# Kernel tuning notes

Hardware: AMD Instinct MI355X
Metric: run time of the kernel (lower is better)

## Reference

```python
import jax, jax.numpy as jnp
import numpy as np

SL, BS, HS, FFN = 2048, 1, 512, 2048
E, TOP_K = 8, 2


def setup_inputs() -> dict:
    key = jax.random.key(0)
    k_x, k_w, k_i, k_w1, k_w2 = jax.random.split(key, 5)
    x = jax.random.normal(k_x, (SL, BS, HS), dtype=jnp.float32)
    expert_weights = jax.random.uniform(k_w, (SL * BS, TOP_K), dtype=jnp.float32)
    expert_indices = jax.random.randint(k_i, (SL * BS, TOP_K), 0, E, dtype=jnp.int32)
    # grouped expert MLP params (megablocks GroupedMLP, regular type, no bias)
    w1 = jax.random.normal(k_w1, (E, HS, FFN), dtype=jnp.float32) * (HS ** -0.5)
    w2 = jax.random.normal(k_w2, (E, FFN, HS), dtype=jnp.float32) * (FFN ** -0.5)
    return {"x": x, "expert_weights": expert_weights, "expert_indices": expert_indices,
            "w1": w1, "w2": w2}


def reference(x, expert_weights, expert_indices, w1, w2):
    sl, bs, hs = x.shape
    n_tok = sl * bs
    xf = x.reshape(n_tok, hs)                      # [N, hs]
    ew = expert_weights.reshape(-1)                # [N*top_k]
    ei = expert_indices.reshape(-1)                # [N*top_k]

    # indices_and_bins: stable radix sort of assignments by expert id
    indices = jnp.argsort(ei)                      # stable in jax -> sorted assignment ids
    bin_ids = ei[indices]                          # sorted expert id per assignment

    # megablocks gather: row for assignment i is indices[i] // top_k
    rows = indices // TOP_K                        # [T]
    xg = xf[rows]                                  # [T, hs] expert-contiguous tokens

    # grouped GEMM expert MLP (dense masked loop over fixed expert count)
    outg = jnp.zeros_like(xg)
    for e in range(E):
        m = (bin_ids == e).astype(x.dtype)[:, None]
        h = jax.nn.gelu(xg @ w1[e], approximate=False)   # [T, ffn]
        outg = outg + m * (h @ w2[e])                    # [T, hs]

    # buffer.index_add_(0, E*input_indices + bin_ids, output.detach())
    buf_idx = E * rows + bin_ids
    buffer = jnp.zeros((n_tok * E, hs), x.dtype).at[buf_idx].add(
        jax.lax.stop_gradient(outg))

    # megablocks scatter: weighted combine back to token order
    y = jnp.zeros((n_tok, hs), x.dtype).at[rows].add(outg * ew[indices][:, None])
    return y.reshape(sl, bs, hs), buffer.reshape(n_tok, E, hs)
```

## Files before the change

kernel.cpp:

```cpp
#include <hip/hip_runtime.h>
#include <hip/hip_bf16.h>

#define NTOK 2048
#define TOPK 2
#define HS   512
#define FFN  2048
#define NE   8
#define TASSIGN (NTOK*TOPK)
#define BM 64
#define PADMAX 4608
#define MAXTILES 72

typedef __attribute__((ext_vector_type(8))) short bf16x8;
typedef __attribute__((ext_vector_type(4))) float f32x4;

static const size_t OFF_XBF  = 0;
static const size_t OFF_WT   = 2097152;
static const size_t OFF_H    = 18874368;
static const size_t OFF_OUTV = 37748736;
static const size_t OFF_RT   = 47185920;
static const size_t OFF_HROF = 47204352;
static const size_t OFF_TE   = 47220736;
static const size_t OFF_TR0  = 47221056;

__device__ __forceinline__ unsigned short f2bf(float f) {
    union { __hip_bfloat16 h; unsigned short u; } v;
    v.h = __float2bfloat16(f);
    return v.u;
}

__device__ __forceinline__ int swz(int r, int byte_off) {
    return byte_off ^ ((r & 7) << 4);
}

__global__ void k_xcvt(const float* __restrict__ x, unsigned short* __restrict__ xbf) {
    int i = (blockIdx.x * 256 + threadIdx.x) * 4;
    float4 v = *(const float4*)(x + i);
    ushort4 o;
    o.x = f2bf(v.x); o.y = f2bf(v.y); o.z = f2bf(v.z); o.w = f2bf(v.w);
    *(ushort4*)(xbf + i) = o;
}

__global__ void k_transpose(const float* __restrict__ in, unsigned short* __restrict__ out,
                            int R, int C) {
    __shared__ unsigned short t[32][33];
    int e = blockIdx.z;
    int rb = blockIdx.y * 32, cb = blockIdx.x * 32;
    int tx = threadIdx.x, ty = threadIdx.y;
    const float* ip = in + (size_t)e * R * C;
    unsigned short* op = out + (size_t)e * C * R;
#pragma unroll
    for (int i = 0; i < 4; i++) {
        int r = ty + i * 8;
        t[r][tx] = f2bf(ip[(size_t)(rb + r) * C + cb + tx]);
    }
    __syncthreads();
#pragma unroll
    for (int i = 0; i < 4; i++) {
        int c = ty + i * 8;
        op[(size_t)(cb + c) * R + rb + tx] = t[tx][c];
    }
}

__global__ void k_setup(const int* __restrict__ ei, const float* __restrict__ ew,
                        int* __restrict__ rowtok, int* __restrict__ hrof,
                        int* __restrict__ tile_e, int* __restrict__ tile_r0) {
    __shared__ int cnt[NE], offpad[NE], cur[NE];
    int tid = threadIdx.x;
    for (int i = tid; i < PADMAX; i += 256) rowtok[i] = -1;
    if (tid < NE) cnt[tid] = 0;
    __syncthreads();
    for (int a = tid; a < TASSIGN; a += 256) atomicAdd(&cnt[ei[a]], 1);
    __syncthreads();
    if (tid == 0) {
        int o = 0, t = 0;
        for (int e = 0; e < NE; e++) {
            offpad[e] = o;
            cur[e] = 0;
            for (int r = 0; r < cnt[e]; r += BM) { tile_e[t] = e; tile_r0[t] = o + r; t++; }
            o += (cnt[e] + BM - 1) / BM * BM;
        }
        for (; t < MAXTILES; t++) { tile_e[t] = -1; tile_r0[t] = 0; }
    }
    __syncthreads();
    for (int a = tid; a < TASSIGN; a += 256) {
        int e = ei[a];
        int r = atomicAdd(&cur[e], 1);
        int hr = offpad[e] + r;
        rowtok[hr] = a >> 1;
        hrof[a] = hr;
    }
}

__global__ __launch_bounds__(256) void k_gemm1(
        const unsigned short* __restrict__ xbf, const unsigned short* __restrict__ w1T,
        unsigned short* __restrict__ H, const int* __restrict__ rowtok,
        const int* __restrict__ tile_e, const int* __restrict__ tile_r0) {
    int mt = blockIdx.y;
    int e = tile_e[mt];
    if (e < 0) return;
    int hr0 = tile_r0[mt];
    int ct = blockIdx.x;

    __shared__ int4 Asv[512];
    __shared__ int4 Bsv[512];
    char* As = (char*)Asv;
    char* Bs = (char*)Bsv;

    int tid = threadIdx.x;
    int lane = tid & 63, wave = tid >> 6;
    int wm = wave >> 1, wn = wave & 1;

    const char* asrc[2]; const char* bsrc[2];
    char* adst[2]; char* bdst[2];
    int atok[2];
#pragma unroll
    for (int p = 0; p < 2; p++) {
        int idx = p * 256 + tid;
        int r = idx >> 3, c8 = idx & 7;
        int token = rowtok[hr0 + r];
        atok[p] = token;
        asrc[p] = (const char*)(xbf + (size_t)(token < 0 ? 0 : token) * HS + c8 * 8);
        bsrc[p] = (const char*)(w1T + ((size_t)e * FFN + ct * 64 + r) * HS + c8 * 8);
        adst[p] = As + swz(r, r * 128 + c8 * 16);
        bdst[p] = Bs + swz(r, r * 128 + c8 * 16);
    }

    f32x4 acc[2][2] = {};
#pragma unroll 1
    for (int kt = 0; kt < HS; kt += 64) {
#pragma unroll
        for (int p = 0; p < 2; p++) {
            int4 va = make_int4(0, 0, 0, 0);
            if (atok[p] >= 0) va = *(const int4*)(asrc[p] + kt * 2);
            *(int4*)adst[p] = va;
            *(int4*)bdst[p] = *(const int4*)(bsrc[p] + kt * 2);
        }
        __syncthreads();
#pragma unroll
        for (int kk = 0; kk < 64; kk += 32) {
            bf16x8 af[2], bfr[2];
#pragma unroll
            for (int f = 0; f < 2; f++) {
                int ar = wm * 32 + f * 16 + (lane & 15);
                af[f] = *(const bf16x8*)(As + swz(ar, ar * 128 + kk * 2 + (lane >> 4) * 16));
                int bc = wn * 32 + f * 16 + (lane & 15);
                bfr[f] = *(const bf16x8*)(Bs + swz(bc, bc * 128 + kk * 2 + (lane >> 4) * 16));
            }
#pragma unroll
            for (int i = 0; i < 2; i++)
#pragma unroll
                for (int j = 0; j < 2; j++)
                    acc[i][j] = __builtin_amdgcn_mfma_f32_16x16x32_bf16(af[i], bfr[j], acc[i][j], 0, 0, 0);
        }
        __syncthreads();
    }
#pragma unroll
    for (int i = 0; i < 2; i++)
#pragma unroll
        for (int j = 0; j < 2; j++)
#pragma unroll
            for (int q = 0; q < 4; q++) {
                int row = wm * 32 + i * 16 + (lane >> 4) * 4 + q;
                int col = ct * 64 + wn * 32 + j * 16 + (lane & 15);
                float v = acc[i][j][q];
                float g = 0.5f * v * (1.0f + erff(v * 0.70710678118f));
                H[(size_t)(hr0 + row) * FFN + col] = f2bf(g);
            }
}

__global__ __launch_bounds__(256) void k_gemm2(
        const unsigned short* __restrict__ H, const unsigned short* __restrict__ w2T,
        float* __restrict__ outv,
        const int* __restrict__ tile_e, const int* __restrict__ tile_r0) {
    int mt = blockIdx.y;
    int e = tile_e[mt];
    if (e < 0) return;
    int hr0 = tile_r0[mt];
    int ct = blockIdx.x;

    __shared__ int4 Asv[512];
    __shared__ int4 Bsv[512];
    char* As = (char*)Asv;
    char* Bs = (char*)Bsv;

    int tid = threadIdx.x;
    int lane = tid & 63, wave = tid >> 6;
    int wm = wave >> 1, wn = wave & 1;

    const char* asrc[2]; const char* bsrc[2];
    char* adst[2]; char* bdst[2];
#pragma unroll
    for (int p = 0; p < 2; p++) {
        int idx = p * 256 + tid;
        int r = idx >> 3, c8 = idx & 7;
        asrc[p] = (const char*)(H + (size_t)(hr0 + r) * FFN + c8 * 8);
        bsrc[p] = (const char*)(w2T + ((size_t)e * HS + ct * 64 + r) * FFN + c8 * 8);
        adst[p] = As + swz(r, r * 128 + c8 * 16);
        bdst[p] = Bs + swz(r, r * 128 + c8 * 16);
    }

    f32x4 acc[2][2] = {};
#pragma unroll 1
    for (int kt = 0; kt < FFN; kt += 64) {
#pragma unroll
        for (int p = 0; p < 2; p++) {
            *(int4*)adst[p] = *(const int4*)(asrc[p] + kt * 2);
            *(int4*)bdst[p] = *(const int4*)(bsrc[p] + kt * 2);
        }
        __syncthreads();
#pragma unroll
        for (int kk = 0; kk < 64; kk += 32) {
            bf16x8 af[2], bfr[2];
#pragma unroll
            for (int f = 0; f < 2; f++) {
                int ar = wm * 32 + f * 16 + (lane & 15);
                af[f] = *(const bf16x8*)(As + swz(ar, ar * 128 + kk * 2 + (lane >> 4) * 16));
                int bc = wn * 32 + f * 16 + (lane & 15);
                bfr[f] = *(const bf16x8*)(Bs + swz(bc, bc * 128 + kk * 2 + (lane >> 4) * 16));
            }
#pragma unroll
            for (int i = 0; i < 2; i++)
#pragma unroll
                for (int j = 0; j < 2; j++)
                    acc[i][j] = __builtin_amdgcn_mfma_f32_16x16x32_bf16(af[i], bfr[j], acc[i][j], 0, 0, 0);
        }
        __syncthreads();
    }
#pragma unroll
    for (int i = 0; i < 2; i++)
#pragma unroll
        for (int j = 0; j < 2; j++)
#pragma unroll
            for (int q = 0; q < 4; q++) {
                int row = wm * 32 + i * 16 + (lane >> 4) * 4 + q;
                int col = ct * 64 + wn * 32 + j * 16 + (lane & 15);
                outv[(size_t)(hr0 + row) * HS + col] = acc[i][j][q];
            }
}

__global__ void k_combine(const float* __restrict__ outv, const int* __restrict__ ei,
                          const float* __restrict__ ew, const int* __restrict__ hrof,
                          float* __restrict__ y, float* __restrict__ buf) {
    int g = blockIdx.x * 256 + threadIdx.x;
    int t = g >> 9, col = g & (HS - 1);
    int a0 = 2 * t, a1 = 2 * t + 1;
    int h0 = hrof[a0], h1 = hrof[a1];
    float o0 = outv[(size_t)h0 * HS + col];
    float o1 = outv[(size_t)h1 * HS + col];
    float w0 = ew[a0], w1 = ew[a1];
    y[g] = w0 * o0 + w1 * o1;
    int e0 = ei[a0], e1 = ei[a1];
    float* bt = buf + (size_t)t * NE * HS + col;
    if (e0 == e1) {
        bt[(size_t)e0 * HS] = o0 + o1;
    } else {
        bt[(size_t)e0 * HS] = o0;
        bt[(size_t)e1 * HS] = o1;
    }
}

extern "C" void kernel_launch(void* const* d_in, const int* in_sizes, int n_in,
                              void* d_out, int out_size, void* d_ws, size_t ws_size,
                              hipStream_t stream) {
    const float* x  = (const float*)d_in[0];
    const float* ew = (const float*)d_in[1];
    const int*   ei = (const int*)d_in[2];
    const float* w1 = (const float*)d_in[3];
    const float* w2 = (const float*)d_in[4];

    char* ws = (char*)d_ws;
    unsigned short* xbf  = (unsigned short*)(ws + OFF_XBF);
    unsigned short* wT   = (unsigned short*)(ws + OFF_WT);
    unsigned short* Hb   = (unsigned short*)(ws + OFF_H);
    float*          outv = (float*)(ws + OFF_OUTV);
    int*            rowtok = (int*)(ws + OFF_RT);
    int*            hrof   = (int*)(ws + OFF_HROF);
    int*            tile_e = (int*)(ws + OFF_TE);
    int*            tile_r0= (int*)(ws + OFF_TR0);

    float* y   = (float*)d_out;
    float* buf = (float*)d_out + (size_t)NTOK * HS;

    hipMemsetAsync(d_out, 0, (size_t)out_size * sizeof(float), stream);

    k_xcvt<<<(NTOK * HS / 4 + 255) / 256, 256, 0, stream>>>(x, xbf);
    k_transpose<<<dim3(FFN / 32, HS / 32, NE), dim3(32, 8), 0, stream>>>(w1, wT, HS, FFN);
    k_setup<<<1, 256, 0, stream>>>(ei, ew, rowtok, hrof, tile_e, tile_r0);
    k_gemm1<<<dim3(FFN / 64, MAXTILES), 256, 0, stream>>>(xbf, wT, Hb, rowtok, tile_e, tile_r0);
    k_transpose<<<dim3(HS / 32, FFN / 32, NE), dim3(32, 8), 0, stream>>>(w2, wT, FFN, HS);
    k_gemm2<<<dim3(HS / 64, MAXTILES), 256, 0, stream>>>(Hb, wT, outv, tile_e, tile_r0);
    k_combine<<<NTOK * HS / 256, 256, 0, stream>>>(outv, ei, ew, hrof, y, buf);
}
```

Baseline: 104.8 us.

## Use direct global-to-LDS loads, larger GEMM tiles, and drop output memset

Merges the two grouped GEMMs into one template that loads A and B tiles straight into LDS via global_load_lds with the XOR swizzle applied on the source side. Tiles grow to 128x128 for the first GEMM and 64x128 for the second, with padding to 128 rows and separate tile lists. The output memset is removed: the combine kernel now writes all eight expert slots per token, and padded rows gather token 0 instead of zero. The two weight transposes go to separate buffers, and the workspace grows.

```diff
diff --git a/kernel.cpp b/kernel.cpp
--- a/kernel.cpp
+++ b/kernel.cpp
@@ -7,21 +7,24 @@
 #define FFN  2048
 #define NE   8
 #define TASSIGN (NTOK*TOPK)
-#define BM 64
-#define PADMAX 4608
-#define MAXTILES 72
+#define PAD  5120
+#define MAXT128 40
+#define MAXT64  72
 
 typedef __attribute__((ext_vector_type(8))) short bf16x8;
 typedef __attribute__((ext_vector_type(4))) float f32x4;
 
 static const size_t OFF_XBF  = 0;
-static const size_t OFF_WT   = 2097152;
-static const size_t OFF_H    = 18874368;
-static const size_t OFF_OUTV = 37748736;
-static const size_t OFF_RT   = 47185920;
-static const size_t OFF_HROF = 47204352;
-static const size_t OFF_TE   = 47220736;
-static const size_t OFF_TR0  = 47221056;
+static const size_t OFF_W1T  = 2097152;
+static const size_t OFF_W2T  = 18874368;
+static const size_t OFF_H    = 35651584;
+static const size_t OFF_OUTV = 56623104;
+static const size_t OFF_RT   = 67108864;
+static const size_t OFF_HROF = 67129344;
+static const size_t OFF_TE128= 67145728;
+static const size_t OFF_TR128= 67145888;
+static const size_t OFF_TE64 = 67146048;
+static const size_t OFF_TR64 = 67146336;
 
 __device__ __forceinline__ unsigned short f2bf(float f) {
     union { __hip_bfloat16 h; unsigned short u; } v;
@@ -32,6 +35,10 @@
 __device__ __forceinline__ int swz(int r, int byte_off) {
     return byte_off ^ ((r & 7) << 4);
 }
+
+#define GLOAD16(gsrc, ldst) \
+    __builtin_amdgcn_global_load_lds((const __attribute__((address_space(1))) void*)(gsrc), \
+                                     (__attribute__((address_space(3))) void*)(ldst), 16, 0, 0)
 
 __global__ void k_xcvt(const float* __restrict__ x, unsigned short* __restrict__ xbf) {
     int i = (blockIdx.x * 256 + threadIdx.x) * 4;
@@ -62,25 +69,27 @@
     }
 }
 
-__global__ void k_setup(const int* __restrict__ ei, const float* __restrict__ ew,
+__global__ void k_setup(const int* __restrict__ ei,
                         int* __restrict__ rowtok, int* __restrict__ hrof,
-                        int* __restrict__ tile_e, int* __restrict__ tile_r0) {
+                        int* __restrict__ te128, int* __restrict__ tr128,
+                        int* __restrict__ te64, int* __restrict__ tr64) {
     __shared__ int cnt[NE], offpad[NE], cur[NE];
     int tid = threadIdx.x;
-    for (int i = tid; i < PADMAX; i += 256) rowtok[i] = -1;
+    for (int i = tid; i < PAD; i += 256) rowtok[i] = 0;
     if (tid < NE) cnt[tid] = 0;
     __syncthreads();
     for (int a = tid; a < TASSIGN; a += 256) atomicAdd(&cnt[ei[a]], 1);
     __syncthreads();
     if (tid == 0) {
-        int o = 0, t = 0;
+        int o = 0, t1 = 0, t2 = 0;
         for (int e = 0; e < NE; e++) {
-            offpad[e] = o;
-            cur[e] = 0;
-            for (int r = 0; r < cnt[e]; r += BM) { tile_e[t] = e; tile_r0[t] = o + r; t++; }
-            o += (cnt[e] + BM - 1) / BM * BM;
+            offpad[e] = o; cur[e] = 0;
+            for (int r = 0; r < cnt[e]; r += 128) { te128[t1] = e; tr128[t1] = o + r; t1++; }
+            for (int r = 0; r < cnt[e]; r += 64)  { te64[t2]  = e; tr64[t2]  = o + r; t2++; }
+            o += (cnt[e] + 127) / 128 * 128;
         }
-        for (; t < MAXTILES; t++) { tile_e[t] = -1; tile_r0[t] = 0; }
+        for (; t1 < MAXT128; t1++) te128[t1] = -1;
+        for (; t2 < MAXT64;  t2++) te64[t2]  = -1;
     }
     __syncthreads();
     for (int a = tid; a < TASSIGN; a += 256) {
@@ -92,151 +101,112 @@
     }
 }
 
-__global__ __launch_bounds__(256) void k_gemm1(
-        const unsigned short* __restrict__ xbf, const unsigned short* __restrict__ w1T,
-        unsigned short* __restrict__ H, const int* __restrict__ rowtok,
-        const int* __restrict__ tile_e, const int* __restrict__ tile_r0) {
+template<int BM, int BN, int K, bool G1>
+__global__ __launch_bounds__(256) void k_gemm(
+        const unsigned short* __restrict__ A,
+        const unsigned short* __restrict__ B,
+        void* __restrict__ outp,
+        const int* __restrict__ rowtok,
+        const int* __restrict__ te, const int* __restrict__ tr) {
+    constexpr int MI = BM / 32;
+    constexpr int NJ = BN / 32;
+    constexpr int PA = BM / 32;
+    constexpr int PB = BN / 32;
     int mt = blockIdx.y;
-    int e = tile_e[mt];
+    int e = te[mt];
     if (e < 0) return;
-    int hr0 = tile_r0[mt];
+    int hr0 = tr[mt];
     int ct = blockIdx.x;
-
-    __shared__ int4 Asv[512];
-    __shared__ int4 Bsv[512];
-    char* As = (char*)Asv;
-    char* Bs = (char*)Bsv;
+    int N = gridDim.x * BN;
+
+    __shared__ unsigned short As[BM * 64];
+    __shared__ unsigned short Bs[BN * 64];
 
     int tid = threadIdx.x;
     int lane = tid & 63, wave = tid >> 6;
     int wm = wave >> 1, wn = wave & 1;
 
-    const char* asrc[2]; const char* bsrc[2];
-    char* adst[2]; char* bdst[2];
-    int atok[2];
-#pragma unroll
-    for (int p = 0; p < 2; p++) {
+    const char* asrc[PA];
+    const char* bsrc[PB];
+#pragma unroll
+    for (int p = 0; p < PA; p++) {
         int idx = p * 256 + tid;
         int r = idx >> 3, c8 = idx & 7;
-        int token = rowtok[hr0 + r];
-        atok[p] = token;
-        asrc[p] = (const char*)(xbf + (size_t)(token < 0 ? 0 : token) * HS + c8 * 8);
-        bsrc[p] = (const char*)(w1T + ((size_t)e * FFN + ct * 64 + r) * HS + c8 * 8);
-        adst[p] = As + swz(r, r * 128 + c8 * 16);
-        bdst[p] = Bs + swz(r, r * 128 + c8 * 16);
-    }
-
-    f32x4 acc[2][2] = {};
+        int c8s = c8 ^ (r & 7);
+        size_t row = G1 ? (size_t)rowtok[hr0 + r] : (size_t)(hr0 + r);
+        asrc[p] = (const char*)(A + row * K) + c8s * 16;
+    }
+#pragma unroll
+    for (int p = 0; p < PB; p++) {
+        int idx = p * 256 + tid;
+        int r = idx >> 3, c8 = idx & 7;
+        int c8s = c8 ^ (r & 7);
+        bsrc[p] = (const char*)(B + ((size_t)e * N + (size_t)ct * BN + r) * K) + c8s * 16;
+    }
+    char* aldst[PA]; char* bldst[PB];
+#pragma unroll
+    for (int p = 0; p < PA; p++) aldst[p] = (char*)As + (p * 256 + wave * 64) * 16;
+#pragma unroll
+    for (int p = 0; p < PB; p++) bldst[p] = (char*)Bs + (p * 256 + wave * 64) * 16;
+
+    f32x4 acc[MI][NJ] = {};
+
 #pragma unroll 1
-    for (int kt = 0; kt < HS; kt += 64) {
-#pragma unroll
-        for (int p = 0; p < 2; p++) {
-            int4 va = make_int4(0, 0, 0, 0);
-            if (atok[p] >= 0) va = *(const int4*)(asrc[p] + kt * 2);
-            *(int4*)adst[p] = va;
-            *(int4*)bdst[p] = *(const int4*)(bsrc[p] + kt * 2);
-        }
+    for (int kt = 0; kt < K; kt += 64) {
+#pragma unroll
+        for (int p = 0; p < PA; p++) GLOAD16(asrc[p] + kt * 2, aldst[p]);
+#pragma unroll
+        for (int p = 0; p < PB; p++) GLOAD16(bsrc[p] + kt * 2, bldst[p]);
         __syncthreads();
 #pragma unroll
         for (int kk = 0; kk < 64; kk += 32) {
-            bf16x8 af[2], bfr[2];
-#pragma unroll
-            for (int f = 0; f < 2; f++) {
-                int ar = wm * 32 + f * 16 + (lane & 15);
-                af[f] = *(const bf16x8*)(As + swz(ar, ar * 128 + kk * 2 + (lane >> 4) * 16));
-                int bc = wn * 32 + f * 16 + (lane & 15);
-                bfr[f] = *(const bf16x8*)(Bs + swz(bc, bc * 128 + kk * 2 + (lane >> 4) * 16));
+            bf16x8 af[MI], bfr[NJ];
+#pragma unroll
+            for (int i = 0; i < MI; i++) {
+                int ar = wm * (BM / 2) + i * 16 + (lane & 15);
+                af[i] = *(const bf16x8*)((const char*)As + swz(ar, ar * 128 + kk * 2 + (lane >> 4) * 16));
             }
 #pragma unroll
-            for (int i = 0; i < 2; i++)
-#pragma unroll
-                for (int j = 0; j < 2; j++)
+            for (int j = 0; j < NJ; j++) {
+                int bc = wn * (BN / 2) + j * 16 + (lane & 15);
+                bfr[j] = *(const bf16x8*)((const char*)Bs + swz(bc, bc * 128 + kk * 2 + (lane >> 4) * 16));
+            }
+#pragma unroll
+            for (int i = 0; i < MI; i++)
+#pragma unroll
+                for (int j = 0; j < NJ; j++)
                     acc[i][j] = __builtin_amdgcn_mfma_f32_16x16x32_bf16(af[i], bfr[j], acc[i][j], 0, 0, 0);
         }
         __syncthreads();
     }
-#pragma unroll
-    for (int i = 0; i < 2; i++)
-#pragma unroll
-        for (int j = 0; j < 2; j++)
-#pragma unroll
-            for (int q = 0; q < 4; q++) {
-                int row = wm * 32 + i * 16 + (lane >> 4) * 4 + q;
-                int col = ct * 64 + wn * 32 + j * 16 + (lane & 15);
-                float v = acc[i][j][q];
-                float g = 0.5f * v * (1.0f + erff(v * 0.70710678118f));
-                H[(size_t)(hr0 + row) * FFN + col] = f2bf(g);
-            }
-}
-
-__global__ __launch_bounds__(256) void k_gemm2(
-        const unsigned short* __restrict__ H, const unsigned short* __restrict__ w2T,
-        float* __restrict__ outv,
-        const int* __restrict__ tile_e, const int* __restrict__ tile_r0) {
-    int mt = blockIdx.y;
-    int e = tile_e[mt];
-    if (e < 0) return;
-    int hr0 = tile_r0[mt];
-    int ct = blockIdx.x;
-
-    __shared__ int4 Asv[512];
-    __shared__ int4 Bsv[512];
-    char* As = (char*)Asv;
-    char* Bs = (char*)Bsv;
-
-    int tid = threadIdx.x;
-    int lane = tid & 63, wave = tid >> 6;
-    int wm = wave >> 1, wn = wave & 1;
-
-    const char* asrc[2]; const char* bsrc[2];
-    char* adst[2]; char* bdst[2];
-#pragma unroll
-    for (int p = 0; p < 2; p++) {
-        int idx = p * 256 + tid;
-        int r = idx >> 3, c8 = idx & 7;
-        asrc[p] = (const char*)(H + (size_t)(hr0 + r) * FFN + c8 * 8);
-        bsrc[p] = (const char*)(w2T + ((size_t)e * HS + ct * 64 + r) * FFN + c8 * 8);
-        adst[p] = As + swz(r, r * 128 + c8 * 16);
-        bdst[p] = Bs + swz(r, r * 128 + c8 * 16);
-    }
-
-    f32x4 acc[2][2] = {};
-#pragma unroll 1
-    for (int kt = 0; kt < FFN; kt += 64) {
-#pragma unroll
-        for (int p = 0; p < 2; p++) {
-            *(int4*)adst[p] = *(const int4*)(asrc[p] + kt * 2);
-            *(int4*)bdst[p] = *(const int4*)(bsrc[p] + kt * 2);
-        }
-        __syncthreads();
-#pragma unroll
-        for (int kk = 0; kk < 64; kk += 32) {
-            bf16x8 af[2], bfr[2];
-#pragma unroll
-            for (int f = 0; f < 2; f++) {
-                int ar = wm * 32 + f * 16 + (lane & 15);
-                af[f] = *(const bf16x8*)(As + swz(ar, ar * 128 + kk * 2 + (lane >> 4) * 16));
-                int bc = wn * 32 + f * 16 + (lane & 15);
-                bfr[f] = *(const bf16x8*)(Bs + swz(bc, bc * 128 + kk * 2 + (lane >> 4) * 16));
-            }
-#pragma unroll
-            for (int i = 0; i < 2; i++)
-#pragma unroll
-                for (int j = 0; j < 2; j++)
-                    acc[i][j] = __builtin_amdgcn_mfma_f32_16x16x32_bf16(af[i], bfr[j], acc[i][j], 0, 0, 0);
-        }
-        __syncthreads();
-    }
-#pragma unroll
-    for (int i = 0; i < 2; i++)
-#pragma unroll
-        for (int j = 0; j < 2; j++)
-#pragma unroll
-            for (int q = 0; q < 4; q++) {
-                int row = wm * 32 + i * 16 + (lane >> 4) * 4 + q;
-                int col = ct * 64 + wn * 32 + j * 16 + (lane & 15);
-                outv[(size_t)(hr0 + row) * HS + col] = acc[i][j][q];
-            }
+
+    if constexpr (G1) {
+        unsigned short* O = (unsigned short*)outp;
+#pragma unroll
+        for (int i = 0; i < MI; i++)
+#pragma unroll
+            for (int j = 0; j < NJ; j++)
+#pragma unroll
+                for (int q = 0; q < 4; q++) {
+                    int row = hr0 + wm * (BM / 2) + i * 16 + (lane >> 4) * 4 + q;
+                    int col = ct * BN + wn * (BN / 2) + j * 16 + (lane & 15);
+                    float v = acc[i][j][q];
+                    float g = 0.5f * v * (1.0f + erff(v * 0.70710678118f));
+                    O[(size_t)row * N + col] = f2bf(g);
+                }
+    } else {
+        float* O = (float*)outp;
+#pragma unroll
+        for (int i = 0; i < MI; i++)
+#pragma unroll
+            for (int j = 0; j < NJ; j++)
+#pragma unroll
+                for (int q = 0; q < 4; q++) {
+                    int row = hr0 + wm * (BM / 2) + i * 16 + (lane >> 4) * 4 + q;
+                    int col = ct * BN + wn * (BN / 2) + j * 16 + (lane & 15);
+                    O[(size_t)row * N + col] = acc[i][j][q];
+                }
+    }
 }
 
 __global__ void k_combine(const float* __restrict__ outv, const int* __restrict__ ei,
@@ -244,19 +214,17 @@
                           float* __restrict__ y, float* __restrict__ buf) {
     int g = blockIdx.x * 256 + threadIdx.x;
     int t = g >> 9, col = g & (HS - 1);
-    int a0 = 2 * t, a1 = 2 * t + 1;
+    int a0 = 2 * t, a1 = a0 + 1;
     int h0 = hrof[a0], h1 = hrof[a1];
     float o0 = outv[(size_t)h0 * HS + col];
     float o1 = outv[(size_t)h1 * HS + col];
-    float w0 = ew[a0], w1 = ew[a1];
-    y[g] = w0 * o0 + w1 * o1;
+    y[g] = ew[a0] * o0 + ew[a1] * o1;
     int e0 = ei[a0], e1 = ei[a1];
-    float* bt = buf + (size_t)t * NE * HS + col;
-    if (e0 == e1) {
-        bt[(size_t)e0 * HS] = o0 + o1;
-    } else {
-        bt[(size_t)e0 * HS] = o0;
-        bt[(size_t)e1 * HS] = o1;
+    float* bt = buf + (size_t)t * (NE * HS) + col;
+#pragma unroll
+    for (int e = 0; e < NE; e++) {
+        float v = (e == e0 ? o0 : 0.0f) + (e == e1 ? o1 : 0.0f);
+        bt[(size_t)e * HS] = v;
     }
 }
 
@@ -271,24 +239,27 @@
 
     char* ws = (char*)d_ws;
     unsigned short* xbf  = (unsigned short*)(ws + OFF_XBF);
-    unsigned short* wT   = (unsigned short*)(ws + OFF_WT);
+    unsigned short* w1T  = (unsigned short*)(ws + OFF_W1T);
+    unsigned short* w2T  = (unsigned short*)(ws + OFF_W2T);
     unsigned short* Hb   = (unsigned short*)(ws + OFF_H);
     float*          outv = (float*)(ws + OFF_OUTV);
     int*            rowtok = (int*)(ws + OFF_RT);
     int*            hrof   = (int*)(ws + OFF_HROF);
-    int*            tile_e = (int*)(ws + OFF_TE);
-    int*            tile_r0= (int*)(ws + OFF_TR0);
+    int*            te128  = (int*)(ws + OFF_TE128);
+    int*            tr128  = (int*)(ws + OFF_TR128);
+    int*            te64   = (int*)(ws + OFF_TE64);
+    int*            tr64   = (int*)(ws + OFF_TR64);
 
     float* y   = (float*)d_out;
     float* buf = (float*)d_out + (size_t)NTOK * HS;
 
-    hipMemsetAsync(d_out, 0, (size_t)out_size * sizeof(float), stream);
-
     k_xcvt<<<(NTOK * HS / 4 + 255) / 256, 256, 0, stream>>>(x, xbf);
-    k_transpose<<<dim3(FFN / 32, HS / 32, NE), dim3(32, 8), 0, stream>>>(w1, wT, HS, FFN);
-    k_setup<<<1, 256, 0, stream>>>(ei, ew, rowtok, hrof, tile_e, tile_r0);
-    k_gemm1<<<dim3(FFN / 64, MAXTILES), 256, 0, stream>>>(xbf, wT, Hb, rowtok, tile_e, tile_r0);
-    k_transpose<<<dim3(HS / 32, FFN / 32, NE), dim3(32, 8), 0, stream>>>(w2, wT, FFN, HS);
-    k_gemm2<<<dim3(HS / 64, MAXTILES), 256, 0, stream>>>(Hb, wT, outv, tile_e, tile_r0);
+    k_transpose<<<dim3(FFN / 32, HS / 32, NE), dim3(32, 8), 0, stream>>>(w1, w1T, HS, FFN);
+    k_transpose<<<dim3(HS / 32, FFN / 32, NE), dim3(32, 8), 0, stream>>>(w2, w2T, FFN, HS);
+    k_setup<<<1, 256, 0, stream>>>(ei, rowtok, hrof, te128, tr128, te64, tr64);
+    k_gemm<128, 128, HS, true><<<dim3(FFN / 128, MAXT128), 256, 0, stream>>>(
+        xbf, w1T, Hb, rowtok, te128, tr128);
+    k_gemm<64, 128, FFN, false><<<dim3(HS / 128, MAXT64), 256, 0, stream>>>(
+        Hb, w2T, outv, rowtok, te64, tr64);
     k_combine<<<NTOK * HS / 256, 256, 0, stream>>>(outv, ei, ew, hrof, y, buf);
 }
```

After: 118.7 us. 13.3% more time.
